# Optimization experiments

Measured on AMD Instinct MI355X. Metric: run time of the kernel, lower is better.

The kernel has to match this reference:

```python
import jax, jax.numpy as jnp
import numpy as np

N_NODES = 50000


def setup_inputs() -> dict:
    key = jax.random.key(0)
    k_x, k_e, k_w1, k_w2 = jax.random.split(key, 4)
    in_c, hid, out_c = 256, 128, 64
    x = jax.random.normal(k_x, (N_NODES, in_c), dtype=jnp.float32)
    edge_index = jax.random.randint(k_e, (2, 800000), 0, N_NODES, dtype=jnp.int64)
    # Glorot-ish scaled weights (faithful to GCNConv default init scale)
    W1 = jax.random.normal(k_w1, (in_c, hid), dtype=jnp.float32) * (1.0 / np.sqrt(in_c))
    b1 = jnp.zeros((hid,), dtype=jnp.float32)
    W2 = jax.random.normal(k_w2, (hid, out_c), dtype=jnp.float32) * (1.0 / np.sqrt(hid))
    b2 = jnp.zeros((out_c,), dtype=jnp.float32)
    return {"x": x, "edge_index": edge_index, "W1": W1, "b1": b1, "W2": W2, "b2": b2}


def _gcn_norm(edge_index, n_nodes):
    # Add self loops, compute symmetric normalization D^-1/2 A D^-1/2.
    loop = jnp.arange(n_nodes, dtype=edge_index.dtype)
    src = jnp.concatenate([edge_index[0], loop])
    dst = jnp.concatenate([edge_index[1], loop])
    deg = jax.ops.segment_sum(jnp.ones_like(dst, dtype=jnp.float32), dst,
                              num_segments=n_nodes)
    dis = jnp.where(deg > 0, jax.lax.rsqrt(deg), 0.0)  # deg_inv_sqrt
    norm = dis[src] * dis[dst]  # [E + N]
    return src, dst, norm


def _gcn_conv(x, W, b, src, dst, norm, n_nodes):
    h = x @ W                                  # [N, F_out] dense transform first
    msgs = h[src] * norm[:, None]              # edge-wise gather + scale
    agg = jax.ops.segment_sum(msgs, dst, num_segments=n_nodes)  # scatter-add
    return agg + b


def reference(x, edge_index, W1, b1, W2, b2):
    n = x.shape[0]
    src, dst, norm = _gcn_norm(edge_index, n)  # cached=True: same norm both layers
    h = _gcn_conv(x, W1, b1, src, dst, norm, n)
    h = jax.nn.relu(h)
    # Dropout is identity in eval mode (deterministic reference)
    return _gcn_conv(h, W2, b2, src, dst, norm, n)
```

## Files before the change

kernel.cpp:

```cpp
#include <hip/hip_runtime.h>


#define IN_C 256
#define HID 128
#define OUTC 64
#define NBLK 256

typedef __attribute__((ext_vector_type(8))) short short8;
typedef __attribute__((ext_vector_type(4))) float f32x4;

__device__ __forceinline__ void gload_lds16(const void* src, void* dst) {
    __builtin_amdgcn_global_load_lds(
        (const __attribute__((address_space(1))) unsigned int*)src,
        (__attribute__((address_space(3))) unsigned int*)dst, 16, 0, 0);
}

__device__ __forceinline__ void bf16split(float f, ushort& h, ushort& l) {
    unsigned u = __float_as_uint(f);
    h = (ushort)(u >> 16);
    float hf = __uint_as_float(u & 0xFFFF0000u);
    unsigned v = __float_as_uint(f - hf);
    l = (ushort)((v + 0x7FFF + ((v >> 16) & 1)) >> 16);
}

__device__ __forceinline__ void cvt8(float4 f0, float4 f1, short8& hi8, short8& lo8) {
    float ff[8];
    *(float4*)&ff[0] = f0; *(float4*)&ff[4] = f1;
    unsigned* hp = (unsigned*)&hi8;
    unsigned* lp = (unsigned*)&lo8;
    #pragma unroll
    for (int i = 0; i < 4; ++i) {
        unsigned u0 = __float_as_uint(ff[2 * i]), u1 = __float_as_uint(ff[2 * i + 1]);
        unsigned hf0 = u0 & 0xFFFF0000u, hf1 = u1 & 0xFFFF0000u;
        hp[i] = (u0 >> 16) | hf1;
        float r0 = ff[2 * i]     - __uint_as_float(hf0);
        float r1 = ff[2 * i + 1] - __uint_as_float(hf1);
        lp[i] = (__float_as_uint(r0) >> 16) | (__float_as_uint(r1) & 0xFFFF0000u);
    }
}

__device__ __forceinline__ ushort f2bf(float f) {
    unsigned u = __float_as_uint(f);
    return (ushort)((u + 0x7FFF + ((u >> 16) & 1)) >> 16);
}
__device__ __forceinline__ float bf2f(ushort u) {
    return __uint_as_float((unsigned)u << 16);
}

__device__ __forceinline__ int edge_at(const void* ei, long long idx, int is32) {
    return is32 ? ((const int*)ei)[idx] : (int)((const long long*)ei)[idx];
}

__device__ __forceinline__ int detect32(const void* ei) {
    const unsigned long long* p = (const unsigned long long*)ei;
    int is32 = 0;
    for (int i = 0; i < 64; ++i)
        if (p[i] >> 32) { is32 = 1; break; }
    return is32;
}

__global__ __launch_bounds__(256) void wtrans_kernel(const float* __restrict__ W1,
                                                     const float* __restrict__ W2,
                                                     ushort* __restrict__ wf1,
                                                     ushort* __restrict__ wf2,
                                                     ushort* __restrict__ h1sent,
                                                     ushort* __restrict__ h2sent) {
    int id = blockIdx.x * 256 + threadIdx.x;
    if (id < 8192) {
        int lane = id & 63, r = id >> 6;
        int pl = r & 1, nt = (r >> 1) & 7, kidx = r >> 4;
        int n = nt * 16 + (lane & 15);
        int kb = kidx * 32 + (lane >> 4) * 8;
        ushort v[8];
        #pragma unroll
        for (int j = 0; j < 8; ++j) {
            ushort h, l; bf16split(W1[(kb + j) * HID + n], h, l);
            v[j] = pl ? l : h;
        }
        *(short8*)&wf1[(size_t)id * 8] = *(short8*)v;
    } else if (id < 10240) {
        int id2 = id - 8192;
        int lane = id2 & 63, r = id2 >> 6;
        int pl = r & 1, nt = (r >> 1) & 3, kidx = r >> 3;
        int n = nt * 16 + (lane & 15);
        int kb = kidx * 32 + (lane >> 4) * 8;
        ushort v[8];
        #pragma unroll
        for (int j = 0; j < 8; ++j) {
            ushort h, l; bf16split(W2[(kb + j) * OUTC + n], h, l);
            v[j] = pl ? l : h;
        }
        *(short8*)&wf2[(size_t)id2 * 8] = *(short8*)v;
    } else if (id < 10368) {
        h1sent[id - 10240] = 0;
    } else if (id < 10432) {
        h2sent[id - 10368] = 0;
    }
}

__global__ __launch_bounds__(256) void bin_count(const void* ei,
                                                 int* __restrict__ blkcnt, int E, int nb) {
    __shared__ int h[256];
    __shared__ int s_is32;
    int t = threadIdx.x;
    h[t] = 0;
    if (t == 0) s_is32 = detect32(ei);
    __syncthreads();
    int is32 = s_is32;
    int chunk = (E + gridDim.x - 1) / gridDim.x;
    long long s0 = (long long)blockIdx.x * chunk;
    long long s1 = s0 + chunk; if (s1 > E) s1 = E;
    for (long long e = s0 + t; e < s1; e += 256) {
        int d = edge_at(ei, (long long)E + e, is32);
        atomicAdd(&h[d >> 8], 1);
    }
    __syncthreads();
    if (t < nb) blkcnt[t * NBLK + blockIdx.x] = h[t];
}

__global__ __launch_bounds__(256) void bin_scan(int* __restrict__ blkcnt,
                                                int* __restrict__ bbase, int nb) {
    __shared__ int sh[256];
    int t = threadIdx.x;
    int tot = 0;
    if (t < nb) {
        int4* p = (int4*)&blkcnt[t * NBLK];
        int run = 0;
        for (int i = 0; i < NBLK / 4; ++i) {
            int4 v = p[i]; int4 o;
            o.x = run; run += v.x; o.y = run; run += v.y;
            o.z = run; run += v.z; o.w = run; run += v.w;
            p[i] = o;
        }
        tot = run;
    }
    sh[t] = tot;
    __syncthreads();
    for (int d = 1; d < 256; d <<= 1) {
        int add = (t >= d) ? sh[t - d] : 0;
        __syncthreads();
        sh[t] += add;
        __syncthreads();
    }
    if (t < nb) {
        bbase[t] = sh[t] - tot;
        if (t == nb - 1) bbase[nb] = sh[t];
    }
}

__global__ __launch_bounds__(256) void bin_scatter(const void* ei,
                                                   const int* __restrict__ blkcnt,
                                                   const int* __restrict__ bbase,
                                                   unsigned* __restrict__ coarse, int E, int nb) {
    __shared__ int cur[256];
    __shared__ int s_is32;
    int t = threadIdx.x;
    if (t < nb) cur[t] = bbase[t] + blkcnt[t * NBLK + blockIdx.x];
    if (t == 0) s_is32 = detect32(ei);
    __syncthreads();
    int is32 = s_is32;
    int chunk = (E + gridDim.x - 1) / gridDim.x;
    long long s0 = (long long)blockIdx.x * chunk;
    long long s1 = s0 + chunk; if (s1 > E) s1 = E;
    for (long long e = s0 + t; e < s1; e += 256) {
        int s = edge_at(ei, e, is32);
        int d = edge_at(ei, (long long)E + e, is32);
        int p = atomicAdd(&cur[d >> 8], 1);
        coarse[p] = (unsigned)s | ((unsigned)(d & 255) << 17);
    }
}

__global__ __launch_bounds__(256) void fine_kernel(const unsigned* __restrict__ coarse,
                                                   const int* __restrict__ bbase,
                                                   int* __restrict__ row_ptr,
                                                   float* __restrict__ dis,
                                                   int* __restrict__ epk,
                                                   int N, int nb, int q1, int q2, int q3) {
    __shared__ int h[1024], cur[1024], ssum[256];
    int b = blockIdx.x, t = threadIdx.x;
    int nb0 = b << 8;
    int e0b = bbase[b], e1b = bbase[b + 1];
    #pragma unroll
    for (int i = 0; i < 4; ++i) h[t + i * 256] = 0;
    __syncthreads();
    for (int e = e0b + t; e < e1b; e += 256) {
        unsigned r = coarse[e];
        int sv = (int)(r & 0x1FFFF);
        int qq = (sv >= q2) ? (sv >= q3 ? 3 : 2) : (sv >= q1 ? 1 : 0);
        atomicAdd(&h[(((r >> 17) & 0xFF) << 2) | qq], 1);
    }
    __syncthreads();
    int v0 = h[4 * t], v1 = h[4 * t + 1], v2 = h[4 * t + 2], v3 = h[4 * t + 3];
    int s = v0 + v1 + v2 + v3;
    ssum[t] = s;
    __syncthreads();
    for (int d = 1; d < 256; d <<= 1) {
        int add = (t >= d) ? ssum[t - d] : 0;
        __syncthreads();
        ssum[t] += add;
        __syncthreads();
    }
    int excl = ssum[t] - s;
    int node = nb0 + t;
    if (node < N) {
        row_ptr[node] = e0b + excl;
        dis[node] = rsqrtf((float)s + 1.0f);
        if (node == N - 1) row_ptr[N] = e0b + ssum[t];
    }
    cur[4 * t] = e0b + excl;
    cur[4 * t + 1] = e0b + excl + v0;
    cur[4 * t + 2] = e0b + excl + v0 + v1;
    cur[4 * t + 3] = e0b + excl + v0 + v1 + v2;
    __syncthreads();
    for (int e = e0b + t; e < e1b; e += 256) {
        unsigned r = coarse[e];
        int sv = (int)(r & 0x1FFFF);
        int qq = (sv >= q2) ? (sv >= q3 ? 3 : 2) : (sv >= q1 ? 1 : 0);
        int p = atomicAdd(&cur[(((r >> 17) & 0xFF) << 2) | qq], 1);
        epk[p] = sv;
    }
}

__global__ __launch_bounds__(256) void gemm1_mfma(const float* __restrict__ X,
                                                  const ushort* __restrict__ wf1,
                                                  const float* __restrict__ dis,
                                                  ushort* __restrict__ HB, int N) {
    __shared__ float xs[64 * 64];
    int t = threadIdx.x;
    int lane = t & 63, w = t >> 6;
    int m_off = (w >> 1) * 32, n_off = (w & 1) * 64;
    long long row0 = (long long)blockIdx.x * 64;
    f32x4 acc[2][4] = {};
    for (int k0i = 0; k0i < 4; ++k0i) {
        __syncthreads();
        #pragma unroll
        for (int i = 0; i < 4; ++i) {
            int lrow = w * 16 + i * 4 + (lane >> 4);
            long long gr = row0 + lrow; if (gr >= N) gr = N - 1;
            int gchunk = (lane & 15) ^ (lrow & 7);
            gload_lds16(X + gr * IN_C + k0i * 64 + gchunk * 4,
                        xs + (w * 16 + i * 4) * 64);
        }
        __syncthreads();
        #pragma unroll
        for (int kk = 0; kk < 2; ++kk) {
            int kidx = k0i * 2 + kk;
            short8 ah[2], al[2], bh[4], bl[4];
            #pragma unroll
            for (int ni = 0; ni < 4; ++ni) {
                int nt = (n_off >> 4) + ni;
                const ushort* bp = wf1 + (size_t)(kidx * 16 + nt * 2) * 512 + lane * 8;
                bh[ni] = *(const short8*)bp;
                bl[ni] = *(const short8*)(bp + 512);
            }
            #pragma unroll
            for (int mi = 0; mi < 2; ++mi) {
                int r = m_off + mi * 16 + (lane & 15);
                int s = r & 7;
                int c0 = kk * 8 + (lane >> 4) * 2;
                float4 f0 = *(float4*)((char*)xs + r * 256 + ((c0 ^ s) * 16));
                float4 f1 = *(float4*)((char*)xs + r * 256 + (((c0 + 1) ^ s) * 16));
                cvt8(f0, f1, ah[mi], al[mi]);
            }
            #pragma unroll
            for (int mi = 0; mi < 2; ++mi)
                #pragma unroll
                for (int ni = 0; ni < 4; ++ni) {
                    acc[mi][ni] = __builtin_amdgcn_mfma_f32_16x16x32_bf16(ah[mi], bh[ni], acc[mi][ni], 0, 0, 0);
                    acc[mi][ni] = __builtin_amdgcn_mfma_f32_16x16x32_bf16(ah[mi], bl[ni], acc[mi][ni], 0, 0, 0);
                    acc[mi][ni] = __builtin_amdgcn_mfma_f32_16x16x32_bf16(al[mi], bh[ni], acc[mi][ni], 0, 0, 0);
                }
        }
    }
    int cr = (lane >> 4) * 4, cc = lane & 15;
    #pragma unroll
    for (int mi = 0; mi < 2; ++mi)
        #pragma unroll
        for (int j = 0; j < 4; ++j) {
            long long gr = row0 + m_off + mi * 16 + cr + j;
            if (gr < N) {
                float dv = dis[gr];
                #pragma unroll
                for (int ni = 0; ni < 4; ++ni) {
                    int col = n_off + ni * 16 + cc;
                    HB[gr * HID + col] = f2bf(acc[mi][ni][j] * dv);
                }
            }
        }
}

__global__ __launch_bounds__(256) void gemm2_mfma(const ushort* __restrict__ Ah,
                                                  const ushort* __restrict__ Al,
                                                  const ushort* __restrict__ wf2,
                                                  const float* __restrict__ dis,
                                                  ushort* __restrict__ HB, int N) {
    __shared__ ushort ash[64 * 64], asl[64 * 64];
    int t = threadIdx.x;
    int lane = t & 63, w = t >> 6;
    int m_off = (w >> 1) * 32, n_off = (w & 1) * 32;
    long long row0 = (long long)blockIdx.x * 64;
    f32x4 acc[2][2] = {};
    for (int k0i = 0; k0i < 2; ++k0i) {
        __syncthreads();
        #pragma unroll
        for (int i = 0; i < 2; ++i) {
            int rbase = w * 16 + i * 8;
            long long gr = row0 + rbase + (lane >> 3);
            size_t so = (size_t)gr * 128 + k0i * 64 + (lane & 7) * 8;
            gload_lds16(Ah + so, ash + rbase * 64);
            gload_lds16(Al + so, asl + rbase * 64);
        }
        __syncthreads();
        #pragma unroll
        for (int kk = 0; kk < 2; ++kk) {
            int kidx = k0i * 2 + kk;
            short8 ah[2], al[2], bh[2], bl[2];
            #pragma unroll
            for (int ni = 0; ni < 2; ++ni) {
                int nt = (n_off >> 4) + ni;
                const ushort* bp = wf2 + (size_t)(kidx * 8 + nt * 2) * 512 + lane * 8;
                bh[ni] = *(const short8*)bp;
                bl[ni] = *(const short8*)(bp + 512);
            }
            #pragma unroll
            for (int mi = 0; mi < 2; ++mi) {
                int r = m_off + mi * 16 + (lane & 15);
                int pos = (kk * 4 + (lane >> 4)) ^ (r & 7);
                ah[mi] = *(short8*)((char*)ash + r * 128 + pos * 16);
                al[mi] = *(short8*)((char*)asl + r * 128 + pos * 16);
            }
            #pragma unroll
            for (int mi = 0; mi < 2; ++mi)
                #pragma unroll
                for (int ni = 0; ni < 2; ++ni) {
                    acc[mi][ni] = __builtin_amdgcn_mfma_f32_16x16x32_bf16(ah[mi], bh[ni], acc[mi][ni], 0, 0, 0);
                    acc[mi][ni] = __builtin_amdgcn_mfma_f32_16x16x32_bf16(ah[mi], bl[ni], acc[mi][ni], 0, 0, 0);
                    acc[mi][ni] = __builtin_amdgcn_mfma_f32_16x16x32_bf16(al[mi], bh[ni], acc[mi][ni], 0, 0, 0);
                }
        }
    }
    int cr = (lane >> 4) * 4, cc = lane & 15;
    #pragma unroll
    for (int mi = 0; mi < 2; ++mi)
        #pragma unroll
        for (int j = 0; j < 4; ++j) {
            long long gr = row0 + m_off + mi * 16 + cr + j;
            if (gr < N) {
                float dv = dis[gr];
                #pragma unroll
                for (int ni = 0; ni < 2; ++ni)
                    HB[gr * OUTC + n_off + ni * 16 + cc] = f2bf(acc[mi][ni][j] * dv);
            }
        }
}

template <int MODE>
__global__ __launch_bounds__(256) void seg_agg_v8(const ushort* __restrict__ H,
                                                  const float* __restrict__ dis,
                                                  const int* __restrict__ row_ptr,
                                                  const int* __restrict__ epk,
                                                  const float* __restrict__ bias,
                                                  float* __restrict__ outF,
                                                  ushort* __restrict__ outH,
                                                  ushort* __restrict__ outL,
                                                  int N) {
    int lane = threadIdx.x & 63;
    int node = (int)(((long long)blockIdx.x * blockDim.x + threadIdx.x) >> 6);
    if (node >= N) return;
    int e0 = row_ptr[node], e1 = row_ptr[node + 1];
    if constexpr (MODE == 0) {
        const unsigned* hl = (const unsigned*)H + lane;
        unsigned v = hl[node * 64];
        float a0 = bf2f((ushort)v), a1 = bf2f((ushort)(v >> 16));
        for (int base = e0; base < e1; base += 64) {
            int cnt = min(64, e1 - base);
            int rec = epk[min(base + lane, e1 - 1)];
            for (int u0 = 0; u0 < cnt; u0 += 16) {
                unsigned hv[16];
                #pragma unroll
                for (int u = 0; u < 16; ++u) {
                    int s = (u0 + u < cnt) ? __builtin_amdgcn_readlane(rec, u0 + u) : N;
                    hv[u] = hl[s * 64];
                }
                #pragma unroll
                for (int u = 0; u < 16; ++u) {
                    a0 += bf2f((ushort)hv[u]);
                    a1 += bf2f((ushort)(hv[u] >> 16));
                }
            }
        }
        float dn = dis[node];
        int c0 = lane * 2;
        float2 bb = *(const float2*)&bias[c0];
        float p0 = fmaxf(dn * a0 + bb.x, 0.f);
        float p1 = fmaxf(dn * a1 + bb.y, 0.f);
        unsigned u0b = __float_as_uint(p0), u1b = __float_as_uint(p1);
        unsigned h0 = u0b >> 16, h1 = u1b >> 16;
        float r0 = p0 - __uint_as_float(u0b & 0xFFFF0000u);
        float r1 = p1 - __uint_as_float(u1b & 0xFFFF0000u);
        unsigned l0 = __float_as_uint(r0) >> 16, l1 = __float_as_uint(r1) >> 16;
        int sl = c0 >> 6, e = c0 & 63;
        int ch = ((e >> 3) ^ (node & 7));
        size_t pos = (size_t)node * 128 + sl * 64 + ch * 8 + (e & 7);
        *(unsigned*)&outH[pos] = h0 | (h1 << 16);
        *(unsigned*)&outL[pos] = l0 | (l1 << 16);
    } else {
        const ushort* hl = H + lane;
        float acc = bf2f(hl[node * 64]);
        for (int base = e0; base < e1; base += 64) {
            int cnt = min(64, e1 - base);
            int rec = epk[min(base + lane, e1 - 1)];
            for (int u0 = 0; u0 < cnt; u0 += 16) {
                float hv[16];
                #pragma unroll
                for (int u = 0; u < 16; ++u) {
                    int s = (u0 + u < cnt) ? __builtin_amdgcn_readlane(rec, u0 + u) : N;
                    hv[u] = bf2f(hl[s * 64]);
                }
                #pragma unroll
                for (int u = 0; u < 16; ++u)
                    acc += hv[u];
            }
        }
        outF[(size_t)node * 64 + lane] = dis[node] * acc + bias[lane];
    }
}

extern "C" void kernel_launch(void* const* d_in, const int* in_sizes, int n_in,
                              void* d_out, int out_size, void* d_ws, size_t ws_size,
                              hipStream_t stream) {
    const float* x  = (const float*)d_in[0];
    const void*  ei = d_in[1];
    const float* W1 = (const float*)d_in[2];
    const float* b1 = (const float*)d_in[3];
    const float* W2 = (const float*)d_in[4];
    const float* b2 = (const float*)d_in[5];
    float* out = (float*)d_out;
    int N = in_sizes[0] / IN_C;
    int E = in_sizes[1] / 2;
    int nb = (N + 255) >> 8;
    int nblk64 = (N + 63) / 64;
    int N_pad = nblk64 * 64;

    char* ws = (char*)d_ws;
    size_t off = 0;
    auto alloc = [&](size_t bytes) {
        void* p = ws + off;
        off += ((bytes + 255) / 256) * 256;
        return p;
    };
    int*      blkcnt  = (int*)alloc((size_t)nb * NBLK * 4);
    int*      bbase   = (int*)alloc(((size_t)nb + 1) * 4);
    int*      row_ptr = (int*)alloc(((size_t)N + 1) * 4);
    float*    dis     = (float*)alloc((size_t)N * 4);
    unsigned* coarse  = (unsigned*)alloc((size_t)E * 4);
    int*      epk     = (int*)alloc((size_t)E * 4);
    ushort*   wf1     = (ushort*)alloc(131072);
    ushort*   wf2     = (ushort*)alloc(32768);
    ushort*   H1b     = (ushort*)alloc(((size_t)N + 1) * HID * 2);
    ushort*   Ah      = (ushort*)alloc((size_t)N_pad * 128 * 2);
    ushort*   Al      = (ushort*)alloc((size_t)N_pad * 128 * 2);
    ushort*   H2b     = (ushort*)alloc(((size_t)N + 1) * OUTC * 2);

    wtrans_kernel<<<41, 256, 0, stream>>>(W1, W2, wf1, wf2,
                                          H1b + (size_t)N * HID,
                                          H2b + (size_t)N * OUTC);
    bin_count<<<NBLK, 256, 0, stream>>>(ei, blkcnt, E, nb);
    bin_scan<<<1, 256, 0, stream>>>(blkcnt, bbase, nb);
    bin_scatter<<<NBLK, 256, 0, stream>>>(ei, blkcnt, bbase, coarse, E, nb);
    fine_kernel<<<nb, 256, 0, stream>>>(coarse, bbase, row_ptr, dis, epk,
                                        N, nb, N / 4, N / 2, (3 * N) / 4);
    gemm1_mfma<<<nblk64, 256, 0, stream>>>(x, wf1, dis, H1b, N);

    int agg_blocks = (int)(((long long)N * 64 + 255) / 256);
    seg_agg_v8<0><<<agg_blocks, 256, 0, stream>>>(H1b, dis, row_ptr, epk,
                                                  b1, nullptr, Ah, Al, N);
    gemm2_mfma<<<nblk64, 256, 0, stream>>>(Ah, Al, wf2, dis, H2b, N);
    seg_agg_v8<1><<<agg_blocks, 256, 0, stream>>>(H2b, dis, row_ptr, epk,
                                                  b2, out, nullptr, nullptr, N);
}
```

Measured before the change: 140.0 us.

## Process 13 nodes per wave in source-quartile phases for gather locality

The aggregation kernels now give each wavefront 13 consecutive nodes and walk their edges in four passes, one per source-index quartile. fine_kernel writes four row pointers per node to support this. The goal is to keep the gathered feature rows within a narrower source range across many waves at the same moment, which should improve L2 hit rate. In exchange, neighbour indices are read one at a time with scalar loads, batched in groups of four instead of sixteen. That leaves fewer loads in flight, and there are about 13x fewer waves, so latency hiding and occupancy may suffer.

```diff
diff --git a/kernel.cpp b/kernel.cpp
--- a/kernel.cpp
+++ b/kernel.cpp
@@ -5,6 +5,7 @@
 #define HID 128
 #define OUTC 64
 #define NBLK 256
+#define KNODES 13
 
 typedef __attribute__((ext_vector_type(8))) short short8;
 typedef __attribute__((ext_vector_type(4))) float f32x4;
@@ -172,7 +173,7 @@
 
 __global__ __launch_bounds__(256) void fine_kernel(const unsigned* __restrict__ coarse,
                                                    const int* __restrict__ bbase,
-                                                   int* __restrict__ row_ptr,
+                                                   int* __restrict__ rp4,
                                                    float* __restrict__ dis,
                                                    int* __restrict__ epk,
                                                    int N, int nb, int q1, int q2, int q3) {
@@ -203,9 +204,13 @@
     int excl = ssum[t] - s;
     int node = nb0 + t;
     if (node < N) {
-        row_ptr[node] = e0b + excl;
+        int b0 = e0b + excl;
+        rp4[node * 4 + 0] = b0;
+        rp4[node * 4 + 1] = b0 + v0;
+        rp4[node * 4 + 2] = b0 + v0 + v1;
+        rp4[node * 4 + 3] = b0 + v0 + v1 + v2;
         dis[node] = rsqrtf((float)s + 1.0f);
-        if (node == N - 1) row_ptr[N] = e0b + ssum[t];
+        if (node == N - 1) rp4[4 * N] = e0b + ssum[t];
     }
     cur[4 * t] = e0b + excl;
     cur[4 * t + 1] = e0b + excl + v0;
@@ -355,9 +360,9 @@
 }
 
 template <int MODE>
-__global__ __launch_bounds__(256) void seg_agg_v8(const ushort* __restrict__ H,
+__global__ __launch_bounds__(256) void seg_agg_v9(const ushort* __restrict__ H,
                                                   const float* __restrict__ dis,
-                                                  const int* __restrict__ row_ptr,
+                                                  const int* __restrict__ rp4,
                                                   const int* __restrict__ epk,
                                                   const float* __restrict__ bias,
                                                   float* __restrict__ outF,
@@ -365,64 +370,101 @@
                                                   ushort* __restrict__ outL,
                                                   int N) {
     int lane = threadIdx.x & 63;
-    int node = (int)(((long long)blockIdx.x * blockDim.x + threadIdx.x) >> 6);
-    if (node >= N) return;
-    int e0 = row_ptr[node], e1 = row_ptr[node + 1];
+    int wv = (int)(((long long)blockIdx.x * blockDim.x + threadIdx.x) >> 6);
+    int n0 = wv * KNODES;
+    if (n0 >= N) return;
     if constexpr (MODE == 0) {
         const unsigned* hl = (const unsigned*)H + lane;
-        unsigned v = hl[node * 64];
-        float a0 = bf2f((ushort)v), a1 = bf2f((ushort)(v >> 16));
-        for (int base = e0; base < e1; base += 64) {
-            int cnt = min(64, e1 - base);
-            int rec = epk[min(base + lane, e1 - 1)];
-            for (int u0 = 0; u0 < cnt; u0 += 16) {
-                unsigned hv[16];
-                #pragma unroll
-                for (int u = 0; u < 16; ++u) {
-                    int s = (u0 + u < cnt) ? __builtin_amdgcn_readlane(rec, u0 + u) : N;
-                    hv[u] = hl[s * 64];
+        float a0[KNODES], a1[KNODES];
+        #pragma unroll
+        for (int i = 0; i < KNODES; ++i) {
+            int n = n0 + i;
+            unsigned v = (n < N) ? hl[(size_t)n * 64] : 0u;
+            a0[i] = bf2f((ushort)v);
+            a1[i] = bf2f((ushort)(v >> 16));
+        }
+        for (int p = 0; p < 4; ++p) {
+            #pragma unroll
+            for (int i = 0; i < KNODES; ++i) {
+                int n = n0 + i;
+                if (n < N) {
+                    int e  = rp4[n * 4 + p];
+                    int ee = rp4[n * 4 + p + 1];
+                    for (; e < ee; e += 4) {
+                        unsigned v[4];
+                        #pragma unroll
+                        for (int j = 0; j < 4; ++j) {
+                            int s = (e + j < ee)
+                                  ? __builtin_amdgcn_readfirstlane(epk[e + j]) : N;
+                            v[j] = hl[(size_t)s * 64];
+                        }
+                        #pragma unroll
+                        for (int j = 0; j < 4; ++j) {
+                            a0[i] += bf2f((ushort)v[j]);
+                            a1[i] += bf2f((ushort)(v[j] >> 16));
+                        }
+                    }
                 }
-                #pragma unroll
-                for (int u = 0; u < 16; ++u) {
-                    a0 += bf2f((ushort)hv[u]);
-                    a1 += bf2f((ushort)(hv[u] >> 16));
-                }
-            }
-        }
-        float dn = dis[node];
+            }
+        }
         int c0 = lane * 2;
         float2 bb = *(const float2*)&bias[c0];
-        float p0 = fmaxf(dn * a0 + bb.x, 0.f);
-        float p1 = fmaxf(dn * a1 + bb.y, 0.f);
-        unsigned u0b = __float_as_uint(p0), u1b = __float_as_uint(p1);
-        unsigned h0 = u0b >> 16, h1 = u1b >> 16;
-        float r0 = p0 - __uint_as_float(u0b & 0xFFFF0000u);
-        float r1 = p1 - __uint_as_float(u1b & 0xFFFF0000u);
-        unsigned l0 = __float_as_uint(r0) >> 16, l1 = __float_as_uint(r1) >> 16;
-        int sl = c0 >> 6, e = c0 & 63;
-        int ch = ((e >> 3) ^ (node & 7));
-        size_t pos = (size_t)node * 128 + sl * 64 + ch * 8 + (e & 7);
-        *(unsigned*)&outH[pos] = h0 | (h1 << 16);
-        *(unsigned*)&outL[pos] = l0 | (l1 << 16);
+        int sl = c0 >> 6, el = c0 & 63;
+        #pragma unroll
+        for (int i = 0; i < KNODES; ++i) {
+            int n = n0 + i;
+            if (n < N) {
+                float dn = dis[n];
+                float p0 = fmaxf(dn * a0[i] + bb.x, 0.f);
+                float p1 = fmaxf(dn * a1[i] + bb.y, 0.f);
+                unsigned u0b = __float_as_uint(p0), u1b = __float_as_uint(p1);
+                unsigned h0 = u0b >> 16, h1 = u1b >> 16;
+                float r0 = p0 - __uint_as_float(u0b & 0xFFFF0000u);
+                float r1 = p1 - __uint_as_float(u1b & 0xFFFF0000u);
+                unsigned l0 = __float_as_uint(r0) >> 16, l1 = __float_as_uint(r1) >> 16;
+                int ch = ((el >> 3) ^ (n & 7));
+                size_t pos = (size_t)n * 128 + sl * 64 + ch * 8 + (el & 7);
+                *(unsigned*)&outH[pos] = h0 | (h1 << 16);
+                *(unsigned*)&outL[pos] = l0 | (l1 << 16);
+            }
+        }
     } else {
         const ushort* hl = H + lane;
-        float acc = bf2f(hl[node * 64]);
-        for (int base = e0; base < e1; base += 64) {
-            int cnt = min(64, e1 - base);
-            int rec = epk[min(base + lane, e1 - 1)];
-            for (int u0 = 0; u0 < cnt; u0 += 16) {
-                float hv[16];
-                #pragma unroll
-                for (int u = 0; u < 16; ++u) {
-                    int s = (u0 + u < cnt) ? __builtin_amdgcn_readlane(rec, u0 + u) : N;
-                    hv[u] = bf2f(hl[s * 64]);
+        float a[KNODES];
+        #pragma unroll
+        for (int i = 0; i < KNODES; ++i) {
+            int n = n0 + i;
+            a[i] = (n < N) ? bf2f(hl[(size_t)n * 64]) : 0.f;
+        }
+        for (int p = 0; p < 4; ++p) {
+            #pragma unroll
+            for (int i = 0; i < KNODES; ++i) {
+                int n = n0 + i;
+                if (n < N) {
+                    int e  = rp4[n * 4 + p];
+                    int ee = rp4[n * 4 + p + 1];
+                    for (; e < ee; e += 4) {
+                        float v[4];
+                        #pragma unroll
+                        for (int j = 0; j < 4; ++j) {
+                            int s = (e + j < ee)
+                                  ? __builtin_amdgcn_readfirstlane(epk[e + j]) : N;
+                            v[j] = bf2f(hl[(size_t)s * 64]);
+                        }
+                        #pragma unroll
+                        for (int j = 0; j < 4; ++j)
+                            a[i] += v[j];
+                    }
                 }
-                #pragma unroll
-                for (int u = 0; u < 16; ++u)
-                    acc += hv[u];
-            }
-        }
-        outF[(size_t)node * 64 + lane] = dis[node] * acc + bias[lane];
+            }
+        }
+        float bv = bias[lane];
+        #pragma unroll
+        for (int i = 0; i < KNODES; ++i) {
+            int n = n0 + i;
+            if (n < N)
+                outF[(size_t)n * 64 + lane] = dis[n] * a[i] + bv;
+        }
     }
 }
 
@@ -451,7 +493,7 @@
     };
     int*      blkcnt  = (int*)alloc((size_t)nb * NBLK * 4);
     int*      bbase   = (int*)alloc(((size_t)nb + 1) * 4);
-    int*      row_ptr = (int*)alloc(((size_t)N + 1) * 4);
+    int*      rp4     = (int*)alloc(((size_t)N * 4 + 1) * 4);
     float*    dis     = (float*)alloc((size_t)N * 4);
     unsigned* coarse  = (unsigned*)alloc((size_t)E * 4);
     int*      epk     = (int*)alloc((size_t)E * 4);
@@ -468,14 +510,15 @@
     bin_count<<<NBLK, 256, 0, stream>>>(ei, blkcnt, E, nb);
     bin_scan<<<1, 256, 0, stream>>>(blkcnt, bbase, nb);
     bin_scatter<<<NBLK, 256, 0, stream>>>(ei, blkcnt, bbase, coarse, E, nb);
-    fine_kernel<<<nb, 256, 0, stream>>>(coarse, bbase, row_ptr, dis, epk,
+    fine_kernel<<<nb, 256, 0, stream>>>(coarse, bbase, rp4, dis, epk,
                                         N, nb, N / 4, N / 2, (3 * N) / 4);
     gemm1_mfma<<<nblk64, 256, 0, stream>>>(x, wf1, dis, H1b, N);
 
-    int agg_blocks = (int)(((long long)N * 64 + 255) / 256);
-    seg_agg_v8<0><<<agg_blocks, 256, 0, stream>>>(H1b, dis, row_ptr, epk,
+    int waves = (N + KNODES - 1) / KNODES;
+    int agg_blocks = (waves + 3) / 4;
+    seg_agg_v9<0><<<agg_blocks, 256, 0, stream>>>(H1b, dis, rp4, epk,
                                                   b1, nullptr, Ah, Al, N);
     gemm2_mfma<<<nblk64, 256, 0, stream>>>(Ah, Al, wf2, dis, H2b, N);
-    seg_agg_v8<1><<<agg_blocks, 256, 0, stream>>>(H2b, dis, row_ptr, epk,
+    seg_agg_v9<1><<<agg_blocks, 256, 0, stream>>>(H2b, dis, rp4, epk,
                                                   b2, out, nullptr, nullptr, N);
 }
```

New measurement: 314.1 us. +124.3%, slower.

## Pad per-node edge lists to multiples of 16 and pack two nodes per wave

Applied to the files above, without the earlier changes.

The fine binning kernel drops the four-way source-quartile sub-sort and pads each node's neighbour list to a multiple of 16, filling the gaps with the sentinel node N, so the aggregation inner loop can skip bounds checks. The row pointer becomes an (offset, padded length) pair. The layer-2 aggregation now handles two 64-feature nodes per wave, one per 32-lane half, using 32-bit loads instead of one 16-bit load per lane. Padding costs extra gathers of the zero row and more epk memory, and removing the quartile sort may weaken gather locality.

```diff
diff --git a/kernel.cpp b/kernel.cpp
--- a/kernel.cpp
+++ b/kernel.cpp
@@ -172,53 +172,44 @@
 
 __global__ __launch_bounds__(256) void fine_kernel(const unsigned* __restrict__ coarse,
                                                    const int* __restrict__ bbase,
-                                                   int* __restrict__ row_ptr,
+                                                   int2* __restrict__ rp2,
                                                    float* __restrict__ dis,
-                                                   int* __restrict__ epk,
-                                                   int N, int nb, int q1, int q2, int q3) {
-    __shared__ int h[1024], cur[1024], ssum[256];
+                                                   int* __restrict__ epk, int N, int nb) {
+    __shared__ int h[256], cur[256], sh[256];
     int b = blockIdx.x, t = threadIdx.x;
     int nb0 = b << 8;
     int e0b = bbase[b], e1b = bbase[b + 1];
-    #pragma unroll
-    for (int i = 0; i < 4; ++i) h[t + i * 256] = 0;
+    int obase0 = e0b + b * 4096;
+    h[t] = 0;
+    __syncthreads();
+    for (int e = e0b + t; e < e1b; e += 256)
+        atomicAdd(&h[(coarse[e] >> 17) & 0xFF], 1);
+    __syncthreads();
+    int cnt = h[t];
+    int pad = (cnt + 15) & ~15;
+    sh[t] = pad;
+    __syncthreads();
+    for (int d = 1; d < 256; d <<= 1) {
+        int add = (t >= d) ? sh[t - d] : 0;
+        __syncthreads();
+        sh[t] += add;
+        __syncthreads();
+    }
+    int base = obase0 + sh[t] - pad;
+    int node = nb0 + t;
+    if (node < N) {
+        rp2[node] = make_int2(base, pad);
+        dis[node] = rsqrtf((float)cnt + 1.0f);
+    }
+    cur[t] = base;
     __syncthreads();
     for (int e = e0b + t; e < e1b; e += 256) {
         unsigned r = coarse[e];
-        int sv = (int)(r & 0x1FFFF);
-        int qq = (sv >= q2) ? (sv >= q3 ? 3 : 2) : (sv >= q1 ? 1 : 0);
-        atomicAdd(&h[(((r >> 17) & 0xFF) << 2) | qq], 1);
-    }
-    __syncthreads();
-    int v0 = h[4 * t], v1 = h[4 * t + 1], v2 = h[4 * t + 2], v3 = h[4 * t + 3];
-    int s = v0 + v1 + v2 + v3;
-    ssum[t] = s;
-    __syncthreads();
-    for (int d = 1; d < 256; d <<= 1) {
-        int add = (t >= d) ? ssum[t - d] : 0;
-        __syncthreads();
-        ssum[t] += add;
-        __syncthreads();
-    }
-    int excl = ssum[t] - s;
-    int node = nb0 + t;
-    if (node < N) {
-        row_ptr[node] = e0b + excl;
-        dis[node] = rsqrtf((float)s + 1.0f);
-        if (node == N - 1) row_ptr[N] = e0b + ssum[t];
-    }
-    cur[4 * t] = e0b + excl;
-    cur[4 * t + 1] = e0b + excl + v0;
-    cur[4 * t + 2] = e0b + excl + v0 + v1;
-    cur[4 * t + 3] = e0b + excl + v0 + v1 + v2;
-    __syncthreads();
-    for (int e = e0b + t; e < e1b; e += 256) {
-        unsigned r = coarse[e];
-        int sv = (int)(r & 0x1FFFF);
-        int qq = (sv >= q2) ? (sv >= q3 ? 3 : 2) : (sv >= q1 ? 1 : 0);
-        int p = atomicAdd(&cur[(((r >> 17) & 0xFF) << 2) | qq], 1);
-        epk[p] = sv;
-    }
+        int p = atomicAdd(&cur[(r >> 17) & 0xFF], 1);
+        epk[p] = (int)(r & 0x1FFFF);
+    }
+    __syncthreads();
+    for (int p = cur[t]; p < base + pad; ++p) epk[p] = N;
 }
 
 __global__ __launch_bounds__(256) void gemm1_mfma(const float* __restrict__ X,
@@ -354,75 +345,112 @@
         }
 }
 
-template <int MODE>
-__global__ __launch_bounds__(256) void seg_agg_v8(const ushort* __restrict__ H,
+__global__ __launch_bounds__(256) void seg_agg_l1(const ushort* __restrict__ H,
                                                   const float* __restrict__ dis,
-                                                  const int* __restrict__ row_ptr,
+                                                  const int2* __restrict__ rp2,
                                                   const int* __restrict__ epk,
                                                   const float* __restrict__ bias,
-                                                  float* __restrict__ outF,
                                                   ushort* __restrict__ outH,
                                                   ushort* __restrict__ outL,
                                                   int N) {
     int lane = threadIdx.x & 63;
     int node = (int)(((long long)blockIdx.x * blockDim.x + threadIdx.x) >> 6);
     if (node >= N) return;
-    int e0 = row_ptr[node], e1 = row_ptr[node + 1];
-    if constexpr (MODE == 0) {
-        const unsigned* hl = (const unsigned*)H + lane;
-        unsigned v = hl[node * 64];
-        float a0 = bf2f((ushort)v), a1 = bf2f((ushort)(v >> 16));
-        for (int base = e0; base < e1; base += 64) {
-            int cnt = min(64, e1 - base);
-            int rec = epk[min(base + lane, e1 - 1)];
-            for (int u0 = 0; u0 < cnt; u0 += 16) {
-                unsigned hv[16];
-                #pragma unroll
-                for (int u = 0; u < 16; ++u) {
-                    int s = (u0 + u < cnt) ? __builtin_amdgcn_readlane(rec, u0 + u) : N;
-                    hv[u] = hl[s * 64];
-                }
-                #pragma unroll
-                for (int u = 0; u < 16; ++u) {
-                    a0 += bf2f((ushort)hv[u]);
-                    a1 += bf2f((ushort)(hv[u] >> 16));
-                }
-            }
-        }
-        float dn = dis[node];
-        int c0 = lane * 2;
-        float2 bb = *(const float2*)&bias[c0];
-        float p0 = fmaxf(dn * a0 + bb.x, 0.f);
-        float p1 = fmaxf(dn * a1 + bb.y, 0.f);
-        unsigned u0b = __float_as_uint(p0), u1b = __float_as_uint(p1);
-        unsigned h0 = u0b >> 16, h1 = u1b >> 16;
-        float r0 = p0 - __uint_as_float(u0b & 0xFFFF0000u);
-        float r1 = p1 - __uint_as_float(u1b & 0xFFFF0000u);
-        unsigned l0 = __float_as_uint(r0) >> 16, l1 = __float_as_uint(r1) >> 16;
-        int sl = c0 >> 6, e = c0 & 63;
-        int ch = ((e >> 3) ^ (node & 7));
-        size_t pos = (size_t)node * 128 + sl * 64 + ch * 8 + (e & 7);
-        *(unsigned*)&outH[pos] = h0 | (h1 << 16);
-        *(unsigned*)&outL[pos] = l0 | (l1 << 16);
-    } else {
-        const ushort* hl = H + lane;
-        float acc = bf2f(hl[node * 64]);
-        for (int base = e0; base < e1; base += 64) {
-            int cnt = min(64, e1 - base);
-            int rec = epk[min(base + lane, e1 - 1)];
-            for (int u0 = 0; u0 < cnt; u0 += 16) {
-                float hv[16];
-                #pragma unroll
-                for (int u = 0; u < 16; ++u) {
-                    int s = (u0 + u < cnt) ? __builtin_amdgcn_readlane(rec, u0 + u) : N;
-                    hv[u] = bf2f(hl[s * 64]);
-                }
-                #pragma unroll
-                for (int u = 0; u < 16; ++u)
-                    acc += hv[u];
-            }
-        }
-        outF[(size_t)node * 64 + lane] = dis[node] * acc + bias[lane];
+    const unsigned* hl = (const unsigned*)H + lane;
+    unsigned v0 = hl[(size_t)node * 64];
+    float a0 = bf2f((ushort)v0), a1 = bf2f((ushort)(v0 >> 16));
+    int2 r2 = rp2[node];
+    int e = r2.x, end = r2.x + r2.y;
+    for (; e < end; e += 64) {
+        int rem = end - e;
+        int rec = epk[min(e + lane, end - 1)];
+        int m = min(64, rem);
+        for (int u0 = 0; u0 < m; u0 += 16) {
+            unsigned hv[16];
+            #pragma unroll
+            for (int u = 0; u < 16; ++u) {
+                int s = __builtin_amdgcn_readlane(rec, u0 + u);
+                hv[u] = hl[(size_t)s * 64];
+            }
+            #pragma unroll
+            for (int u = 0; u < 16; ++u) {
+                a0 += bf2f((ushort)hv[u]);
+                a1 += bf2f((ushort)(hv[u] >> 16));
+            }
+        }
+    }
+    float dn = dis[node];
+    int c0 = lane * 2;
+    float2 bb = *(const float2*)&bias[c0];
+    float p0 = fmaxf(dn * a0 + bb.x, 0.f);
+    float p1 = fmaxf(dn * a1 + bb.y, 0.f);
+    unsigned u0b = __float_as_uint(p0), u1b = __float_as_uint(p1);
+    unsigned h0 = u0b >> 16, h1 = u1b >> 16;
+    float r0 = p0 - __uint_as_float(u0b & 0xFFFF0000u);
+    float r1 = p1 - __uint_as_float(u1b & 0xFFFF0000u);
+    unsigned l0 = __float_as_uint(r0) >> 16, l1 = __float_as_uint(r1) >> 16;
+    int sl = c0 >> 6, el = c0 & 63;
+    int ch = ((el >> 3) ^ (node & 7));
+    size_t pos = (size_t)node * 128 + sl * 64 + ch * 8 + (el & 7);
+    *(unsigned*)&outH[pos] = h0 | (h1 << 16);
+    *(unsigned*)&outL[pos] = l0 | (l1 << 16);
+}
+
+__global__ __launch_bounds__(256) void seg_agg_l2(const ushort* __restrict__ H,
+                                                  const float* __restrict__ dis,
+                                                  const int2* __restrict__ rp2,
+                                                  const int* __restrict__ epk,
+                                                  const float* __restrict__ bias,
+                                                  float* __restrict__ outF,
+                                                  int N) {
+    int lane = threadIdx.x & 63;
+    int wv = (int)(((long long)blockIdx.x * blockDim.x + threadIdx.x) >> 6);
+    int n0 = wv * 2;
+    if (n0 >= N) return;
+    int n1 = n0 + 1;
+    int has1 = (n1 < N);
+    int half = lane >> 5;
+    int myn = half ? (has1 ? n1 : N) : n0;
+    int f2 = (lane & 31) * 2;
+    unsigned v0 = *(const unsigned*)&H[(size_t)myn * 64 + f2];
+    float a0 = bf2f((ushort)v0), a1 = bf2f((ushort)(v0 >> 16));
+    int2 rA = rp2[n0];
+    int2 rB = has1 ? rp2[n1] : make_int2(0, 0);
+    int eA = rA.x, endA = rA.x + rA.y;
+    int eB = rB.x, endB = rB.x + rB.y;
+    while (eA < endA || eB < endB) {
+        int remA = endA - eA, remB = endB - eB;
+        int mA = remA > 0 ? min(64, remA) : 0;
+        int mB = remB > 0 ? min(64, remB) : 0;
+        int recA = mA ? epk[min(eA + lane, endA - 1)] : 0;
+        int recB = mB ? epk[min(eB + lane, endB - 1)] : 0;
+        int m = max(mA, mB);
+        for (int u0 = 0; u0 < m; u0 += 16) {
+            unsigned hv[16];
+            #pragma unroll
+            for (int u = 0; u < 16; ++u) {
+                int idx = u0 + u;
+                int sA = (idx < mA) ? __builtin_amdgcn_readlane(recA, idx) : N;
+                int sB = (idx < mB) ? __builtin_amdgcn_readlane(recB, idx) : N;
+                int s = half ? sB : sA;
+                hv[u] = *(const unsigned*)&H[(size_t)s * 64 + f2];
+            }
+            #pragma unroll
+            for (int u = 0; u < 16; ++u) {
+                a0 += bf2f((ushort)hv[u]);
+                a1 += bf2f((ushort)(hv[u] >> 16));
+            }
+        }
+        eA += mA; eB += mB;
+    }
+    if (!half || has1) {
+        int sn = half ? n1 : n0;
+        float dn = dis[sn];
+        float2 bb = *(const float2*)&bias[f2];
+        float2 o;
+        o.x = dn * a0 + bb.x;
+        o.y = dn * a1 + bb.y;
+        *(float2*)&outF[(size_t)sn * 64 + f2] = o;
     }
 }
 
@@ -451,10 +479,10 @@
     };
     int*      blkcnt  = (int*)alloc((size_t)nb * NBLK * 4);
     int*      bbase   = (int*)alloc(((size_t)nb + 1) * 4);
-    int*      row_ptr = (int*)alloc(((size_t)N + 1) * 4);
+    int2*     rp2     = (int2*)alloc((size_t)N * 8);
     float*    dis     = (float*)alloc((size_t)N * 4);
     unsigned* coarse  = (unsigned*)alloc((size_t)E * 4);
-    int*      epk     = (int*)alloc((size_t)E * 4);
+    int*      epk     = (int*)alloc(((size_t)E + (size_t)nb * 4096) * 4);
     ushort*   wf1     = (ushort*)alloc(131072);
     ushort*   wf2     = (ushort*)alloc(32768);
     ushort*   H1b     = (ushort*)alloc(((size_t)N + 1) * HID * 2);
@@ -468,14 +496,13 @@
     bin_count<<<NBLK, 256, 0, stream>>>(ei, blkcnt, E, nb);
     bin_scan<<<1, 256, 0, stream>>>(blkcnt, bbase, nb);
     bin_scatter<<<NBLK, 256, 0, stream>>>(ei, blkcnt, bbase, coarse, E, nb);
-    fine_kernel<<<nb, 256, 0, stream>>>(coarse, bbase, row_ptr, dis, epk,
-                                        N, nb, N / 4, N / 2, (3 * N) / 4);
+    fine_kernel<<<nb, 256, 0, stream>>>(coarse, bbase, rp2, dis, epk, N, nb);
     gemm1_mfma<<<nblk64, 256, 0, stream>>>(x, wf1, dis, H1b, N);
 
-    int agg_blocks = (int)(((long long)N * 64 + 255) / 256);
-    seg_agg_v8<0><<<agg_blocks, 256, 0, stream>>>(H1b, dis, row_ptr, epk,
-                                                  b1, nullptr, Ah, Al, N);
+    int agg1_blocks = (int)(((long long)N * 64 + 255) / 256);
+    seg_agg_l1<<<agg1_blocks, 256, 0, stream>>>(H1b, dis, rp2, epk, b1, Ah, Al, N);
     gemm2_mfma<<<nblk64, 256, 0, stream>>>(Ah, Al, wf2, dis, H2b, N);
-    seg_agg_v8<1><<<agg_blocks, 256, 0, stream>>>(H2b, dis, row_ptr, epk,
-                                                  b2, out, nullptr, nullptr, N);
-}
+    int waves2 = (N + 1) / 2;
+    int agg2_blocks = (int)(((long long)waves2 * 64 + 255) / 256);
+    seg_agg_l2<<<agg2_blocks, 256, 0, stream>>>(H2b, dis, rp2, epk, b2, out, N);
+}
```

Result: no change. 139.0 us, median of 2 (-0.8%).
